# Kernel tuning notes

Hardware: AMD Instinct MI355X
Metric: run time of the kernel (lower is better)

The kernel has to match this reference:

```python
import jax, jax.numpy as jnp
import numpy as np

N = 50000
E = 800000
H = 128
L = 3
EPS_BN = 1e-5
EPS_NORM = 1e-12
NEG_SLOPE = 0.1


def setup_inputs() -> dict:
    key = jax.random.key(0)
    ks = jax.random.split(key, 10)
    s = 1.0 / np.sqrt(H)
    x = jax.random.normal(ks[0], (N, H), dtype=jnp.float32)
    edge_index = jax.random.randint(ks[1], (2, E), 0, N, dtype=jnp.int64)
    # per-layer SAGEConv params: lin_l (neighbors, with bias), lin_r (root, no bias)
    Wl = jax.random.uniform(ks[2], (L, H, H), jnp.float32, -s, s)
    bl = jax.random.uniform(ks[3], (L, H), jnp.float32, -s, s)
    Wr = jax.random.uniform(ks[4], (L, H, H), jnp.float32, -s, s)
    # BatchNorm affine params per layer
    gamma = jnp.ones((L, H), jnp.float32)
    beta = jnp.zeros((L, H), jnp.float32)
    # shared skip linear
    Ws = jax.random.uniform(ks[5], (H, H), jnp.float32, -s, s)
    bs = jax.random.uniform(ks[6], (H,), jnp.float32, -s, s)
    return {"x": x, "edge_index": edge_index, "Wl": Wl, "bl": bl, "Wr": Wr,
            "gamma": gamma, "beta": beta, "Ws": Ws, "bs": bs}


def _layer(x, src, dst, Wl, bl, Wr, g, b, Ws, bs):
    # skip residual
    res = x @ Ws.T + bs
    # SAGEConv mean aggregation: messages src -> dst
    agg = jax.ops.segment_sum(x[src], dst, num_segments=N)  # [N,H]
    deg = jax.ops.segment_sum(jnp.ones((E,), x.dtype), dst, num_segments=N)
    agg = agg / jnp.maximum(deg, 1.0)[:, None]
    out = agg @ Wl.T + bl + x @ Wr.T
    # normalize=True -> L2 normalize over features
    nrm = jnp.sqrt(jnp.sum(out * out, axis=-1, keepdims=True))
    out = out / jnp.maximum(nrm, EPS_NORM)
    # BatchNorm over nodes (batch statistics)
    mu = out.mean(axis=0)
    var = out.var(axis=0)
    out = (out - mu) * jax.lax.rsqrt(var + EPS_BN) * g + b
    # LeakyReLU(0.1); dropout is identity in eval
    out = jnp.where(out >= 0, out, NEG_SLOPE * out)
    return out + res


def reference(x, edge_index, Wl, bl, Wr, gamma, beta, Ws, bs):
    src, dst = edge_index[0], edge_index[1]
    for l in range(L):
        x = _layer(x, src, dst, Wl[l], bl[l], Wr[l], gamma[l], beta[l], Ws, bs)
    return x
```

## Files before the change

### kernel.cpp

```cpp
#include <hip/hip_runtime.h>
#include <hip/hip_bf16.h>
#include <stdint.h>

#define NN 50000
#define NE 800000
#define HD 128
#define NL 3
#define EPS_BN 1e-5f
#define EPS_NORM 1e-12f
#define NEG_SLOPE 0.1f

#define SCAN_CHUNK 256
#define SCAN_BLOCKS ((NN + SCAN_CHUNK - 1) / SCAN_CHUNK)
#define NTILES ((NN + 127) / 128)

#define BSH 9
#define NB ((NN + (1 << BSH) - 1) >> BSH)
#define MAXBE 9728

typedef __attribute__((ext_vector_type(8))) short bf16x8;
typedef __attribute__((ext_vector_type(4))) float f32x4;

static __device__ __forceinline__ unsigned pack_bf16(float a, float b) {
  unsigned ua = __builtin_bit_cast(unsigned, a);
  unsigned ub = __builtin_bit_cast(unsigned, b);
  ua = (ua + 0x7fffu + ((ua >> 16) & 1u)) >> 16;
  ub = (ub + 0x7fffu + ((ub >> 16) & 1u)) >> 16;
  return ua | (ub << 16);
}
static __device__ __forceinline__ ushort bf16of(float f) {
  unsigned u = __builtin_bit_cast(unsigned, f);
  u = (u + 0x7fffu + ((u >> 16) & 1u)) >> 16;
  return (ushort)u;
}
static __device__ __forceinline__ float bflo(unsigned u) { return __builtin_bit_cast(float, u << 16); }
static __device__ __forceinline__ float bfhi(unsigned u) { return __builtin_bit_cast(float, u & 0xffff0000u); }

__global__ __launch_bounds__(256) void hist_kernel(const int* __restrict__ dst, int* __restrict__ degi) {
  int i = blockIdx.x * 256 + threadIdx.x;
  if (i < NE) atomicAdd(&degi[dst[i]], 1);
}

__global__ __launch_bounds__(256) void blocksum_kernel(const int* __restrict__ degi,
                                                       int* __restrict__ blocksum) {
  __shared__ int sh[256];
  int t = threadIdx.x;
  int i = blockIdx.x * 256 + t;
  sh[t] = (i < NN) ? degi[i] : 0;
  __syncthreads();
  for (int off = 128; off >= 1; off >>= 1) {
    if (t < off) sh[t] += sh[t + off];
    __syncthreads();
  }
  if (t == 0) blocksum[blockIdx.x] = sh[0];
}

__global__ __launch_bounds__(256) void blockscan_kernel(int* __restrict__ blocksum,
                                                        int* __restrict__ blockoff,
                                                        int* __restrict__ rowptr) {
  __shared__ int sh[256];
  int t = threadIdx.x;
  int v = (t < SCAN_BLOCKS) ? blocksum[t] : 0;
  sh[t] = v;
  __syncthreads();
  for (int off = 1; off < 256; off <<= 1) {
    int u = (t >= off) ? sh[t - off] : 0;
    __syncthreads();
    sh[t] += u;
    __syncthreads();
  }
  if (t < SCAN_BLOCKS) blockoff[t] = sh[t] - v;
  if (t == 255) rowptr[NN] = sh[255];
}

__global__ __launch_bounds__(256) void chunkscan_kernel(const int* __restrict__ degi,
                                                        const int* __restrict__ blockoff,
                                                        int* __restrict__ rowptr,
                                                        int* __restrict__ bcursor,
                                                        float* __restrict__ invdeg) {
  __shared__ int sh[256];
  int t = threadIdx.x;
  int i = blockIdx.x * 256 + t;
  int d = (i < NN) ? degi[i] : 0;
  sh[t] = d;
  __syncthreads();
  for (int off = 1; off < 256; off <<= 1) {
    int u = (t >= off) ? sh[t - off] : 0;
    __syncthreads();
    sh[t] += u;
    __syncthreads();
  }
  if (i < NN) {
    int pre = blockoff[blockIdx.x] + sh[t] - d;
    rowptr[i] = pre;
    if ((i & ((1 << BSH) - 1)) == 0) bcursor[i >> BSH] = pre;
    invdeg[i] = 1.0f / fmaxf((float)d, 1.0f);
  }
}

__global__ __launch_bounds__(1024) void bucketB_kernel(const int* __restrict__ src,
                                                       const int* __restrict__ dst,
                                                       int* __restrict__ bcursor,
                                                       uint2* __restrict__ bpack) {
  __shared__ int hist[NB], lstart[NB], gbase[NB];
  __shared__ uint2 sdat[1024];
  const int tid = threadIdx.x;
  const int e = blockIdx.x * 1024 + tid;
  if (tid < NB) hist[tid] = 0;
  __syncthreads();
  int s = 0, d = 0, b = 0, myIdx = 0;
  bool valid = (e < NE);
  if (valid) {
    s = src[e];
    d = dst[e];
    b = d >> BSH;
    myIdx = atomicAdd(&hist[b], 1);
  }
  __syncthreads();
  if (tid == 0) {
    int run = 0;
    for (int i = 0; i < NB; ++i) { lstart[i] = run; run += hist[i]; }
  }
  __syncthreads();
  if (tid < NB && hist[tid] > 0) gbase[tid] = atomicAdd(&bcursor[tid], hist[tid]);
  __syncthreads();
  if (valid) sdat[lstart[b] + myIdx] = make_uint2((unsigned)s, (unsigned)d);
  __syncthreads();
  int tot = lstart[NB - 1] + hist[NB - 1];
  if (tid < tot) {
    uint2 p = sdat[tid];
    int bb = (int)(p.y >> BSH);
    bpack[gbase[bb] + (tid - lstart[bb])] = p;
  }
}

__global__ __launch_bounds__(1024) void bucketC_kernel(const int* __restrict__ rowptr,
                                                       const uint2* __restrict__ bpack,
                                                       int* __restrict__ esrc) {
  __shared__ int lcur[1 << BSH];
  __shared__ int lsrc[MAXBE];
  const int c = blockIdx.x, tid = threadIdx.x;
  const int nbase = c << BSH;
  const int nend = min(nbase + (1 << BSH), NN);
  const int ebase = rowptr[nbase];
  const int cnt = rowptr[nend] - ebase;
  if (tid < (1 << BSH)) {
    int n = nbase + tid;
    lcur[tid] = (n < nend) ? rowptr[n] - ebase : 0;
  }
  __syncthreads();
  for (int i = tid; i < cnt; i += 1024) {
    uint2 p = bpack[ebase + i];
    int pos = atomicAdd(&lcur[(int)p.y - nbase], 1);
    if (pos < MAXBE) lsrc[pos] = (int)p.x;
  }
  __syncthreads();
  for (int i = tid; i < cnt; i += 1024) esrc[ebase + i] = lsrc[i];
}

__global__ __launch_bounds__(256) void tobf16_kernel(const float* __restrict__ x, ushort* __restrict__ xb) {
  int i = blockIdx.x * 256 + threadIdx.x;
  if (i < NN * 64) {
    float2 f = *(const float2*)(x + (size_t)i * 2);
    *(unsigned*)(xb + (size_t)i * 2) = pack_bf16(f.x, f.y);
  }
}

__global__ __launch_bounds__(256) void packW_kernel(const float* __restrict__ Wl,
                                                    const float* __restrict__ Wr,
                                                    const float* __restrict__ Wsm,
                                                    unsigned* __restrict__ wpackL,
                                                    unsigned* __restrict__ wpackS) {
  int i = blockIdx.x * 256 + threadIdx.x;
  if (i < NL * 16384) {
    int l = i >> 14, rem = i & 16383;
    int c = rem >> 7, kp = rem & 127;
    int k2 = kp * 2;
    float f0, f1;
    if (k2 < HD) { const float* W = Wl + (size_t)l * HD * HD + c * HD + k2; f0 = W[0]; f1 = W[1]; }
    else         { const float* W = Wr + (size_t)l * HD * HD + c * HD + (k2 - HD); f0 = W[0]; f1 = W[1]; }
    unsigned ba = (unsigned)(c * 512 + kp * 4) ^ (unsigned)((c & 7) << 4);
    *(unsigned*)((char*)(wpackL + (size_t)l * 16384) + ba) = pack_bf16(f0, f1);
  } else if (i < NL * 16384 + 8192) {
    int j = i - NL * 16384;
    int c = j >> 6, kp = j & 63;
    int k2 = kp * 2;
    unsigned ba = (unsigned)(c * 256 + kp * 4) ^ (unsigned)((c & 7) << 4);
    *(unsigned*)((char*)wpackS + ba) = pack_bf16(Wsm[c * HD + k2], Wsm[c * HD + k2 + 1]);
  }
}

__global__ __launch_bounds__(512) void agg_csr_kernel(const ushort* __restrict__ xb,
                                                      const int* __restrict__ rowptr,
                                                      const int* __restrict__ esrc,
                                                      const float* __restrict__ invdeg,
                                                      ushort* __restrict__ aggb,
                                                      float* __restrict__ colsum,
                                                      float* __restrict__ colsumsq) {
  if (blockIdx.x == 0 && threadIdx.x < 2 * HD) {
    if (threadIdx.x < HD) colsum[threadIdx.x] = 0.f;
    else colsumsq[threadIdx.x - HD] = 0.f;
  }
  int wid = (blockIdx.x * 512 + threadIdx.x) >> 6;
  int lane = threadIdx.x & 63;
  int half = lane >> 5, sub = lane & 31;
  int node = wid * 2 + half;
  if (node >= NN) return;
  int start = rowptr[node], end = rowptr[node + 1];
  float a0 = 0.f, a1 = 0.f, a2 = 0.f, a3 = 0.f;
  int e = start;
  for (; e + 4 <= end; e += 4) {
    int s0 = esrc[e], s1 = esrc[e + 1], s2 = esrc[e + 2], s3 = esrc[e + 3];
    uint2 u0 = *(const uint2*)((const char*)xb + (size_t)s0 * 256 + sub * 8);
    uint2 u1 = *(const uint2*)((const char*)xb + (size_t)s1 * 256 + sub * 8);
    uint2 u2 = *(const uint2*)((const char*)xb + (size_t)s2 * 256 + sub * 8);
    uint2 u3 = *(const uint2*)((const char*)xb + (size_t)s3 * 256 + sub * 8);
    a0 += (bflo(u0.x) + bflo(u1.x)) + (bflo(u2.x) + bflo(u3.x));
    a1 += (bfhi(u0.x) + bfhi(u1.x)) + (bfhi(u2.x) + bfhi(u3.x));
    a2 += (bflo(u0.y) + bflo(u1.y)) + (bflo(u2.y) + bflo(u3.y));
    a3 += (bfhi(u0.y) + bfhi(u1.y)) + (bfhi(u2.y) + bfhi(u3.y));
  }
  for (; e < end; ++e) {
    uint2 u = *(const uint2*)((const char*)xb + (size_t)esrc[e] * 256 + sub * 8);
    a0 += bflo(u.x);
    a1 += bfhi(u.x);
    a2 += bflo(u.y);
    a3 += bfhi(u.y);
  }
  float id = invdeg[node];
  uint2 o;
  o.x = pack_bf16(a0 * id, a1 * id);
  o.y = pack_bf16(a2 * id, a3 * id);
  *(uint2*)((char*)aggb + (size_t)node * 256 + sub * 8) = o;
}

__global__ __launch_bounds__(512, 4) void mfma_pre_kernel(
    const ushort* __restrict__ aggb, const ushort* __restrict__ xb,
    const unsigned* __restrict__ wpackL, const float* __restrict__ bl,
    uint4* __restrict__ prebn,
    float* __restrict__ colsum, float* __restrict__ colsumsq) {
  __shared__ unsigned Bsw[16384];
  __shared__ float lsum[HD], lsq[HD];
  const int tid = threadIdx.x;
  {
    const uint4* s = (const uint4*)wpackL;
    uint4* d = (uint4*)Bsw;
#pragma unroll
    for (int i = 0; i < 8; ++i) d[tid + i * 512] = s[tid + i * 512];
  }
  if (tid < HD) { lsum[tid] = 0.f; lsq[tid] = 0.f; }

  const int wave = tid >> 6, lane = tid & 63;
  const int lhi = lane >> 4, llo = lane & 15;
  int arow = blockIdx.x * 128 + wave * 16 + llo;
  if (arow >= NN) arow = NN - 1;
  const size_t rb = (size_t)arow * 256;

  uint4 areg[8];
#pragma unroll
  for (int ks = 0; ks < 4; ++ks) {
    areg[ks]     = *(const uint4*)((const char*)aggb + rb + ks * 64 + lhi * 16);
    areg[ks + 4] = *(const uint4*)((const char*)xb   + rb + ks * 64 + lhi * 16);
  }

  f32x4 acc[8];
#pragma unroll
  for (int ct = 0; ct < 8; ++ct) {
    float b = bl[ct * 16 + llo];
    acc[ct] = (f32x4){b, b, b, b};
  }
  __syncthreads();

#pragma unroll
  for (int ks = 0; ks < 8; ++ks) {
    bf16x8 a = __builtin_bit_cast(bf16x8, areg[ks]);
#pragma unroll
    for (int ct = 0; ct < 8; ++ct) {
      int bcol = ct * 16 + llo;
      unsigned bb = (unsigned)(bcol * 512 + ks * 64 + lhi * 16) ^ (unsigned)((bcol & 7) << 4);
      bf16x8 b = *(const bf16x8*)((const char*)Bsw + bb);
      acc[ct] = __builtin_amdgcn_mfma_f32_16x16x32_bf16(a, b, acc[ct], 0, 0, 0);
    }
  }

  float cs[8] = {0, 0, 0, 0, 0, 0, 0, 0}, cq[8] = {0, 0, 0, 0, 0, 0, 0, 0};
#pragma unroll
  for (int r = 0; r < 4; ++r) {
    int orow = blockIdx.x * 128 + wave * 16 + lhi * 4 + r;
    float p[8];
    float ss = 0.f;
#pragma unroll
    for (int ct = 0; ct < 8; ++ct) { p[ct] = acc[ct][r]; ss += p[ct] * p[ct]; }
#pragma unroll
    for (int m = 8; m >= 1; m >>= 1) ss += __shfl_xor(ss, m, 64);
    float inv = 1.0f / fmaxf(sqrtf(ss), EPS_NORM);
#pragma unroll
    for (int ct = 0; ct < 8; ++ct) p[ct] *= inv;
    uint4 o;
    o.x = pack_bf16(p[0], p[1]);
    o.y = pack_bf16(p[2], p[3]);
    o.z = pack_bf16(p[4], p[5]);
    o.w = pack_bf16(p[6], p[7]);
    prebn[((size_t)blockIdx.x * 32 + wave * 4 + r) * 64 + lane] = o;
    if (orow < NN) {
#pragma unroll
      for (int ct = 0; ct < 8; ++ct) { cs[ct] += p[ct]; cq[ct] += p[ct] * p[ct]; }
    }
  }
#pragma unroll
  for (int ct = 0; ct < 8; ++ct) {
    atomicAdd(&lsum[ct * 16 + llo], cs[ct]);
    atomicAdd(&lsq[ct * 16 + llo], cq[ct]);
  }
  __syncthreads();
  if (tid < HD) {
    atomicAdd(&colsum[tid], lsum[tid]);
    atomicAdd(&colsumsq[tid], lsq[tid]);
  }
}

__global__ __launch_bounds__(512, 4) void res_mfma_kernel(
    ushort* __restrict__ xb, const uint4* __restrict__ prebn,
    const unsigned* __restrict__ wpackS, const float* __restrict__ bs,
    const float* __restrict__ colsum, const float* __restrict__ colsumsq,
    const float* __restrict__ gamma, const float* __restrict__ beta,
    float* __restrict__ outf, int last) {
  __shared__ unsigned Bsw[8192];
  __shared__ float lscale[HD], lshift[HD];
  const int tid = threadIdx.x;
  {
    const uint4* s = (const uint4*)wpackS;
    uint4* d = (uint4*)Bsw;
#pragma unroll
    for (int i = 0; i < 4; ++i) d[tid + i * 512] = s[tid + i * 512];
  }
  if (tid < HD) {
    float mu = colsum[tid] * (1.0f / NN);
    float ex2 = colsumsq[tid] * (1.0f / NN);
    float var = ex2 - mu * mu;
    float sc = gamma[tid] * rsqrtf(var + EPS_BN);
    lscale[tid] = sc;
    lshift[tid] = beta[tid] - mu * sc;
  }

  const int wave = tid >> 6, lane = tid & 63;
  const int lhi = lane >> 4, llo = lane & 15;
  int arow = blockIdx.x * 128 + wave * 16 + llo;
  if (arow >= NN) arow = NN - 1;
  const size_t rb = (size_t)arow * 256;

  uint4 areg[4];
#pragma unroll
  for (int ks = 0; ks < 4; ++ks)
    areg[ks] = *(const uint4*)((const char*)xb + rb + ks * 64 + lhi * 16);
  uint4 pv4[4];
#pragma unroll
  for (int r = 0; r < 4; ++r)
    pv4[r] = prebn[((size_t)blockIdx.x * 32 + wave * 4 + r) * 64 + lane];

  f32x4 acc[8];
#pragma unroll
  for (int ct = 0; ct < 8; ++ct) {
    float b = bs[ct * 16 + llo];
    acc[ct] = (f32x4){b, b, b, b};
  }
  __syncthreads();

  float sc8[8], sh8[8];
#pragma unroll
  for (int ct = 0; ct < 8; ++ct) {
    int C = ct * 16 + llo;
    sc8[ct] = lscale[C];
    sh8[ct] = lshift[C];
  }

#pragma unroll
  for (int ks = 0; ks < 4; ++ks) {
    bf16x8 a = __builtin_bit_cast(bf16x8, areg[ks]);
#pragma unroll
    for (int ct = 0; ct < 8; ++ct) {
      int bcol = ct * 16 + llo;
      unsigned bb = (unsigned)(bcol * 256 + ks * 64 + lhi * 16) ^ (unsigned)((bcol & 7) << 4);
      bf16x8 b = *(const bf16x8*)((const char*)Bsw + bb);
      acc[ct] = __builtin_amdgcn_mfma_f32_16x16x32_bf16(a, b, acc[ct], 0, 0, 0);
    }
  }

#pragma unroll
  for (int r = 0; r < 4; ++r) {
    int orow = blockIdx.x * 128 + wave * 16 + lhi * 4 + r;
    if (orow < NN) {
      const unsigned* pw = (const unsigned*)&pv4[r];
#pragma unroll
      for (int ct = 0; ct < 8; ++ct) {
        unsigned w = pw[ct >> 1];
        float pv = (ct & 1) ? bfhi(w) : bflo(w);
        float v = pv * sc8[ct] + sh8[ct];
        v = v >= 0.f ? v : NEG_SLOPE * v;
        float o = v + acc[ct][r];
        if (last) outf[(size_t)orow * HD + ct * 16 + llo] = o;
        else      xb[(size_t)orow * HD + ct * 16 + llo] = bf16of(o);
      }
    }
  }
}

extern "C" void kernel_launch(void* const* d_in, const int* in_sizes, int n_in,
                              void* d_out, int out_size, void* d_ws, size_t ws_size,
                              hipStream_t stream) {
  const float* x0    = (const float*)d_in[0];
  const int*   ei    = (const int*)d_in[1];
  const float* Wl    = (const float*)d_in[2];
  const float* bl    = (const float*)d_in[3];
  const float* Wr    = (const float*)d_in[4];
  const float* gamma = (const float*)d_in[5];
  const float* beta  = (const float*)d_in[6];
  const float* Wsm   = (const float*)d_in[7];
  const float* bs    = (const float*)d_in[8];
  float* out = (float*)d_out;

  char* w = (char*)d_ws;
  ushort* aggb = (ushort*)w;        w += (size_t)NN * HD * 2;
  ushort* xb   = (ushort*)w;        w += (size_t)NN * HD * 2;
  uint4* prebn = (uint4*)w;         w += (size_t)NTILES * 32 * 64 * 16;
  unsigned* wpackL = (unsigned*)w;  w += (size_t)NL * 16384 * 4;
  unsigned* wpackS = (unsigned*)w;  w += 8192 * 4;
  float* invdeg = (float*)w;        w += (size_t)NN * 4;
  float* colsum = (float*)w;        w += HD * 4;
  float* colsumsq = (float*)w;      w += HD * 4;
  int* degi = (int*)w;              w += (size_t)NN * 4;
  int* rowptr = (int*)w;            w += (size_t)(NN + 1) * 4;
  int* bcursor = (int*)w;           w += (size_t)(NB + 8) * 4;
  int* blocksum = (int*)w;          w += SCAN_BLOCKS * 4;
  int* blockoff = (int*)w;          w += SCAN_BLOCKS * 4;
  uint2* bpack = (uint2*)w;         w += (size_t)NE * 8;
  int* esrc = (int*)w;              w += (size_t)NE * 4;

  const int* srcp = ei;
  const int* dstp = ei + NE;

  hipMemsetAsync(degi, 0, NN * sizeof(int), stream);
  hist_kernel<<<(NE + 255) / 256, 256, 0, stream>>>(dstp, degi);
  blocksum_kernel<<<SCAN_BLOCKS, 256, 0, stream>>>(degi, blocksum);
  blockscan_kernel<<<1, 256, 0, stream>>>(blocksum, blockoff, rowptr);
  chunkscan_kernel<<<SCAN_BLOCKS, 256, 0, stream>>>(degi, blockoff, rowptr, bcursor, invdeg);
  bucketB_kernel<<<(NE + 1023) / 1024, 1024, 0, stream>>>(srcp, dstp, bcursor, bpack);
  bucketC_kernel<<<NB, 1024, 0, stream>>>(rowptr, bpack, esrc);
  tobf16_kernel<<<(NN * 64 + 255) / 256, 256, 0, stream>>>(x0, xb);
  packW_kernel<<<(NL * 16384 + 8192 + 255) / 256, 256, 0, stream>>>(Wl, Wr, Wsm, wpackL, wpackS);

  const int aggBlocks = ((NN + 1) / 2 * 64 + 511) / 512;
  for (int l = 0; l < NL; ++l) {
    agg_csr_kernel<<<aggBlocks, 512, 0, stream>>>(xb, rowptr, esrc, invdeg, aggb,
                                                  colsum, colsumsq);
    mfma_pre_kernel<<<NTILES, 512, 0, stream>>>(aggb, xb, wpackL + (size_t)l * 16384,
                                                bl + (size_t)l * HD, prebn, colsum, colsumsq);
    res_mfma_kernel<<<NTILES, 512, 0, stream>>>(xb, prebn, wpackS, bs,
                                                colsum, colsumsq,
                                                gamma + (size_t)l * HD, beta + (size_t)l * HD,
                                                out, l == NL - 1 ? 1 : 0);
  }
}
```

Baseline: 317.6 us.

## Fuse prep kernels, merge scan with last-block ticket, degree-sort aggregation nodes

Merges the degree histogram, bf16 conversion of x and weight packing into one multi-role prep kernel. Folds the block-sum and block-scan kernels into one, where the last block to finish (found with an atomic ticket) does the scan. Adds a single-block counting sort of nodes by degree so each wavefront aggregates nodes of similar degree. The aggregation kernel now uses 16 lanes per node with 16-byte loads, so each wavefront covers 4 nodes. This cuts launch count and load imbalance, at the cost of an extra serial single-block sort and an indirection through perm.

Measured after the change: 339.7 us. +7.0%, slower.

```diff
diff --git a/kernel.cpp b/kernel.cpp
--- a/kernel.cpp
+++ b/kernel.cpp
@@ -18,6 +18,11 @@
 #define NB ((NN + (1 << BSH) - 1) >> BSH)
 #define MAXBE 9728
 
+#define PREP_HIST_B ((NE + 255) / 256)
+#define PREP_TOB_B  ((NN * 64 + 255) / 256)
+#define PREP_PACK_B ((NL * 16384 + 8192 + 255) / 256)
+#define PREP_TOTAL_B (PREP_HIST_B + PREP_TOB_B + PREP_PACK_B)
+
 typedef __attribute__((ext_vector_type(8))) short bf16x8;
 typedef __attribute__((ext_vector_type(4))) float f32x4;
 
@@ -36,14 +41,55 @@
 static __device__ __forceinline__ float bflo(unsigned u) { return __builtin_bit_cast(float, u << 16); }
 static __device__ __forceinline__ float bfhi(unsigned u) { return __builtin_bit_cast(float, u & 0xffff0000u); }
 
-__global__ __launch_bounds__(256) void hist_kernel(const int* __restrict__ dst, int* __restrict__ degi) {
-  int i = blockIdx.x * 256 + threadIdx.x;
-  if (i < NE) atomicAdd(&degi[dst[i]], 1);
-}
-
-__global__ __launch_bounds__(256) void blocksum_kernel(const int* __restrict__ degi,
-                                                       int* __restrict__ blocksum) {
+__global__ __launch_bounds__(256) void prep_kernel(const int* __restrict__ dst,
+                                                   const float* __restrict__ x,
+                                                   const float* __restrict__ Wl,
+                                                   const float* __restrict__ Wr,
+                                                   const float* __restrict__ Wsm,
+                                                   int* __restrict__ degi,
+                                                   ushort* __restrict__ xb,
+                                                   unsigned* __restrict__ wpackL,
+                                                   unsigned* __restrict__ wpackS,
+                                                   int* __restrict__ done_counter) {
+  int b = blockIdx.x;
+  if (b == 0 && threadIdx.x == 0) *done_counter = 0;
+  if (b < PREP_HIST_B) {
+    int i = b * 256 + threadIdx.x;
+    if (i < NE) atomicAdd(&degi[dst[i]], 1);
+  } else if (b < PREP_HIST_B + PREP_TOB_B) {
+    int i = (b - PREP_HIST_B) * 256 + threadIdx.x;
+    if (i < NN * 64) {
+      float2 f = *(const float2*)(x + (size_t)i * 2);
+      *(unsigned*)(xb + (size_t)i * 2) = pack_bf16(f.x, f.y);
+    }
+  } else {
+    int i = (b - PREP_HIST_B - PREP_TOB_B) * 256 + threadIdx.x;
+    if (i < NL * 16384) {
+      int l = i >> 14, rem = i & 16383;
+      int c = rem >> 7, kp = rem & 127;
+      int k2 = kp * 2;
+      float f0, f1;
+      if (k2 < HD) { const float* W = Wl + (size_t)l * HD * HD + c * HD + k2; f0 = W[0]; f1 = W[1]; }
+      else         { const float* W = Wr + (size_t)l * HD * HD + c * HD + (k2 - HD); f0 = W[0]; f1 = W[1]; }
+      unsigned ba = (unsigned)(c * 512 + kp * 4) ^ (unsigned)((c & 7) << 4);
+      *(unsigned*)((char*)(wpackL + (size_t)l * 16384) + ba) = pack_bf16(f0, f1);
+    } else if (i < NL * 16384 + 8192) {
+      int j = i - NL * 16384;
+      int c = j >> 6, kp = j & 63;
+      int k2 = kp * 2;
+      unsigned ba = (unsigned)(c * 256 + kp * 4) ^ (unsigned)((c & 7) << 4);
+      *(unsigned*)((char*)wpackS + ba) = pack_bf16(Wsm[c * HD + k2], Wsm[c * HD + k2 + 1]);
+    }
+  }
+}
+
+__global__ __launch_bounds__(256) void bsum_scan_kernel(const int* __restrict__ degi,
+                                                        int* __restrict__ blocksum,
+                                                        int* __restrict__ blockoff,
+                                                        int* __restrict__ rowptr,
+                                                        int* __restrict__ done_counter) {
   __shared__ int sh[256];
+  __shared__ int lastflag;
   int t = threadIdx.x;
   int i = blockIdx.x * 256 + t;
   sh[t] = (i < NN) ? degi[i] : 0;
@@ -52,25 +98,26 @@
     if (t < off) sh[t] += sh[t + off];
     __syncthreads();
   }
-  if (t == 0) blocksum[blockIdx.x] = sh[0];
-}
-
-__global__ __launch_bounds__(256) void blockscan_kernel(int* __restrict__ blocksum,
-                                                        int* __restrict__ blockoff,
-                                                        int* __restrict__ rowptr) {
-  __shared__ int sh[256];
-  int t = threadIdx.x;
-  int v = (t < SCAN_BLOCKS) ? blocksum[t] : 0;
-  sh[t] = v;
-  __syncthreads();
-  for (int off = 1; off < 256; off <<= 1) {
-    int u = (t >= off) ? sh[t - off] : 0;
+  if (t == 0) {
+    blocksum[blockIdx.x] = sh[0];
+    __threadfence();
+    int ticket = atomicAdd(done_counter, 1);
+    lastflag = (ticket == SCAN_BLOCKS - 1) ? 1 : 0;
+  }
+  __syncthreads();
+  if (lastflag) {
+    int v = (t < SCAN_BLOCKS) ? blocksum[t] : 0;
+    sh[t] = v;
     __syncthreads();
-    sh[t] += u;
-    __syncthreads();
-  }
-  if (t < SCAN_BLOCKS) blockoff[t] = sh[t] - v;
-  if (t == 255) rowptr[NN] = sh[255];
+    for (int off = 1; off < 256; off <<= 1) {
+      int u = (t >= off) ? sh[t - off] : 0;
+      __syncthreads();
+      sh[t] += u;
+      __syncthreads();
+    }
+    if (t < SCAN_BLOCKS) blockoff[t] = sh[t] - v;
+    if (t == 255) rowptr[NN] = sh[255];
+  }
 }
 
 __global__ __launch_bounds__(256) void chunkscan_kernel(const int* __restrict__ degi,
@@ -95,6 +142,27 @@
     rowptr[i] = pre;
     if ((i & ((1 << BSH) - 1)) == 0) bcursor[i >> BSH] = pre;
     invdeg[i] = 1.0f / fmaxf((float)d, 1.0f);
+  }
+}
+
+__global__ __launch_bounds__(1024) void degsort_kernel(const int* __restrict__ degi,
+                                                       int* __restrict__ perm) {
+  __shared__ int bins[64];
+  __shared__ int base[64];
+  int t = threadIdx.x;
+  if (t < 64) bins[t] = 0;
+  __syncthreads();
+  for (int i = t; i < NN; i += 1024) atomicAdd(&bins[min(degi[i], 63)], 1);
+  __syncthreads();
+  if (t == 0) {
+    int run = 0;
+    for (int b = 0; b < 64; ++b) { base[b] = run; run += bins[b]; bins[b] = 0; }
+  }
+  __syncthreads();
+  for (int i = t; i < NN; i += 1024) {
+    int b = min(degi[i], 63);
+    int pos = base[b] + atomicAdd(&bins[b], 1);
+    perm[pos] = i;
   }
 }
 
@@ -158,42 +226,11 @@
   for (int i = tid; i < cnt; i += 1024) esrc[ebase + i] = lsrc[i];
 }
 
-__global__ __launch_bounds__(256) void tobf16_kernel(const float* __restrict__ x, ushort* __restrict__ xb) {
-  int i = blockIdx.x * 256 + threadIdx.x;
-  if (i < NN * 64) {
-    float2 f = *(const float2*)(x + (size_t)i * 2);
-    *(unsigned*)(xb + (size_t)i * 2) = pack_bf16(f.x, f.y);
-  }
-}
-
-__global__ __launch_bounds__(256) void packW_kernel(const float* __restrict__ Wl,
-                                                    const float* __restrict__ Wr,
-                                                    const float* __restrict__ Wsm,
-                                                    unsigned* __restrict__ wpackL,
-                                                    unsigned* __restrict__ wpackS) {
-  int i = blockIdx.x * 256 + threadIdx.x;
-  if (i < NL * 16384) {
-    int l = i >> 14, rem = i & 16383;
-    int c = rem >> 7, kp = rem & 127;
-    int k2 = kp * 2;
-    float f0, f1;
-    if (k2 < HD) { const float* W = Wl + (size_t)l * HD * HD + c * HD + k2; f0 = W[0]; f1 = W[1]; }
-    else         { const float* W = Wr + (size_t)l * HD * HD + c * HD + (k2 - HD); f0 = W[0]; f1 = W[1]; }
-    unsigned ba = (unsigned)(c * 512 + kp * 4) ^ (unsigned)((c & 7) << 4);
-    *(unsigned*)((char*)(wpackL + (size_t)l * 16384) + ba) = pack_bf16(f0, f1);
-  } else if (i < NL * 16384 + 8192) {
-    int j = i - NL * 16384;
-    int c = j >> 6, kp = j & 63;
-    int k2 = kp * 2;
-    unsigned ba = (unsigned)(c * 256 + kp * 4) ^ (unsigned)((c & 7) << 4);
-    *(unsigned*)((char*)wpackS + ba) = pack_bf16(Wsm[c * HD + k2], Wsm[c * HD + k2 + 1]);
-  }
-}
-
 __global__ __launch_bounds__(512) void agg_csr_kernel(const ushort* __restrict__ xb,
                                                       const int* __restrict__ rowptr,
                                                       const int* __restrict__ esrc,
                                                       const float* __restrict__ invdeg,
+                                                      const int* __restrict__ perm,
                                                       ushort* __restrict__ aggb,
                                                       float* __restrict__ colsum,
                                                       float* __restrict__ colsumsq) {
@@ -203,35 +240,42 @@
   }
   int wid = (blockIdx.x * 512 + threadIdx.x) >> 6;
   int lane = threadIdx.x & 63;
-  int half = lane >> 5, sub = lane & 31;
-  int node = wid * 2 + half;
-  if (node >= NN) return;
+  int slot = wid * 4 + (lane >> 4);
+  int sub = lane & 15;
+  if (slot >= NN) return;
+  int node = perm[slot];
   int start = rowptr[node], end = rowptr[node + 1];
-  float a0 = 0.f, a1 = 0.f, a2 = 0.f, a3 = 0.f;
+  float a0 = 0.f, a1 = 0.f, a2 = 0.f, a3 = 0.f, a4 = 0.f, a5 = 0.f, a6 = 0.f, a7 = 0.f;
   int e = start;
   for (; e + 4 <= end; e += 4) {
     int s0 = esrc[e], s1 = esrc[e + 1], s2 = esrc[e + 2], s3 = esrc[e + 3];
-    uint2 u0 = *(const uint2*)((const char*)xb + (size_t)s0 * 256 + sub * 8);
-    uint2 u1 = *(const uint2*)((const char*)xb + (size_t)s1 * 256 + sub * 8);
-    uint2 u2 = *(const uint2*)((const char*)xb + (size_t)s2 * 256 + sub * 8);
-    uint2 u3 = *(const uint2*)((const char*)xb + (size_t)s3 * 256 + sub * 8);
+    uint4 u0 = *(const uint4*)((const char*)xb + (size_t)s0 * 256 + sub * 16);
+    uint4 u1 = *(const uint4*)((const char*)xb + (size_t)s1 * 256 + sub * 16);
+    uint4 u2 = *(const uint4*)((const char*)xb + (size_t)s2 * 256 + sub * 16);
+    uint4 u3 = *(const uint4*)((const char*)xb + (size_t)s3 * 256 + sub * 16);
     a0 += (bflo(u0.x) + bflo(u1.x)) + (bflo(u2.x) + bflo(u3.x));
     a1 += (bfhi(u0.x) + bfhi(u1.x)) + (bfhi(u2.x) + bfhi(u3.x));
     a2 += (bflo(u0.y) + bflo(u1.y)) + (bflo(u2.y) + bflo(u3.y));
     a3 += (bfhi(u0.y) + bfhi(u1.y)) + (bfhi(u2.y) + bfhi(u3.y));
+    a4 += (bflo(u0.z) + bflo(u1.z)) + (bflo(u2.z) + bflo(u3.z));
+    a5 += (bfhi(u0.z) + bfhi(u1.z)) + (bfhi(u2.z) + bfhi(u3.z));
+    a6 += (bflo(u0.w) + bflo(u1.w)) + (bflo(u2.w) + bflo(u3.w));
+    a7 += (bfhi(u0.w) + bfhi(u1.w)) + (bfhi(u2.w) + bfhi(u3.w));
   }
   for (; e < end; ++e) {
-    uint2 u = *(const uint2*)((const char*)xb + (size_t)esrc[e] * 256 + sub * 8);
-    a0 += bflo(u.x);
-    a1 += bfhi(u.x);
-    a2 += bflo(u.y);
-    a3 += bfhi(u.y);
+    uint4 u = *(const uint4*)((const char*)xb + (size_t)esrc[e] * 256 + sub * 16);
+    a0 += bflo(u.x); a1 += bfhi(u.x);
+    a2 += bflo(u.y); a3 += bfhi(u.y);
+    a4 += bflo(u.z); a5 += bfhi(u.z);
+    a6 += bflo(u.w); a7 += bfhi(u.w);
   }
   float id = invdeg[node];
-  uint2 o;
+  uint4 o;
   o.x = pack_bf16(a0 * id, a1 * id);
   o.y = pack_bf16(a2 * id, a3 * id);
-  *(uint2*)((char*)aggb + (size_t)node * 256 + sub * 8) = o;
+  o.z = pack_bf16(a4 * id, a5 * id);
+  o.w = pack_bf16(a6 * id, a7 * id);
+  *(uint4*)((char*)aggb + (size_t)node * 256 + sub * 16) = o;
 }
 
 __global__ __launch_bounds__(512, 4) void mfma_pre_kernel(
@@ -430,9 +474,11 @@
   float* colsumsq = (float*)w;      w += HD * 4;
   int* degi = (int*)w;              w += (size_t)NN * 4;
   int* rowptr = (int*)w;            w += (size_t)(NN + 1) * 4;
+  int* perm = (int*)w;              w += (size_t)NN * 4;
   int* bcursor = (int*)w;           w += (size_t)(NB + 8) * 4;
   int* blocksum = (int*)w;          w += SCAN_BLOCKS * 4;
   int* blockoff = (int*)w;          w += SCAN_BLOCKS * 4;
+  int* done_counter = (int*)w;      w += 16;
   uint2* bpack = (uint2*)w;         w += (size_t)NE * 8;
   int* esrc = (int*)w;              w += (size_t)NE * 4;
 
@@ -440,18 +486,18 @@
   const int* dstp = ei + NE;
 
   hipMemsetAsync(degi, 0, NN * sizeof(int), stream);
-  hist_kernel<<<(NE + 255) / 256, 256, 0, stream>>>(dstp, degi);
-  blocksum_kernel<<<SCAN_BLOCKS, 256, 0, stream>>>(degi, blocksum);
-  blockscan_kernel<<<1, 256, 0, stream>>>(blocksum, blockoff, rowptr);
+  prep_kernel<<<PREP_TOTAL_B, 256, 0, stream>>>(dstp, x0, Wl, Wr, Wsm,
+                                                degi, xb, wpackL, wpackS, done_counter);
+  bsum_scan_kernel<<<SCAN_BLOCKS, 256, 0, stream>>>(degi, blocksum, blockoff, rowptr,
+                                                    done_counter);
   chunkscan_kernel<<<SCAN_BLOCKS, 256, 0, stream>>>(degi, blockoff, rowptr, bcursor, invdeg);
+  degsort_kernel<<<1, 1024, 0, stream>>>(degi, perm);
   bucketB_kernel<<<(NE + 1023) / 1024, 1024, 0, stream>>>(srcp, dstp, bcursor, bpack);
   bucketC_kernel<<<NB, 1024, 0, stream>>>(rowptr, bpack, esrc);
-  tobf16_kernel<<<(NN * 64 + 255) / 256, 256, 0, stream>>>(x0, xb);
-  packW_kernel<<<(NL * 16384 + 8192 + 255) / 256, 256, 0, stream>>>(Wl, Wr, Wsm, wpackL, wpackS);
-
-  const int aggBlocks = ((NN + 1) / 2 * 64 + 511) / 512;
+
+  const int aggBlocks = (((NN + 3) / 4) * 64 + 511) / 512;
   for (int l = 0; l < NL; ++l) {
-    agg_csr_kernel<<<aggBlocks, 512, 0, stream>>>(xb, rowptr, esrc, invdeg, aggb,
+    agg_csr_kernel<<<aggBlocks, 512, 0, stream>>>(xb, rowptr, esrc, invdeg, perm, aggb,
                                                   colsum, colsumsq);
     mfma_pre_kernel<<<NTILES, 512, 0, stream>>>(aggb, xb, wpackL + (size_t)l * 16384,
                                                 bl + (size_t)l * HD, prebn, colsum, colsumsq);
```
